# Performance work log

Measured on AMD Instinct MI355X. Metric: run time of the kernel, lower is better.

Reference implementation:

```python
import jax, jax.numpy as jnp
import numpy as np

N_NODES = 100000
N_EDGES = 800000
IN_DIM, HID_DIM, OUT_DIM = 128, 64, 7


def setup_inputs() -> dict:
    key = jax.random.key(0)
    ks = jax.random.split(key, 8)
    x = jax.random.normal(ks[0], (N_NODES, IN_DIM), dtype=jnp.float32)
    edge_index = jax.random.randint(ks[1], (2, N_EDGES), 0, N_NODES, dtype=jnp.int64)
    # Glorot-ish init for weights, zeros for bias (PyG GCNConv default)
    def glorot(k, shape):
        lim = float(np.sqrt(6.0 / (shape[0] + shape[1])))
        return jax.random.uniform(k, shape, dtype=jnp.float32, minval=-lim, maxval=lim)
    return {
        "x": x,
        "edge_index": edge_index,
        "W1": glorot(ks[2], (IN_DIM, HID_DIM)),
        "b1": jnp.zeros((HID_DIM,), jnp.float32),
        "W2": glorot(ks[3], (HID_DIM, HID_DIM)),
        "b2": jnp.zeros((HID_DIM,), jnp.float32),
        "W3": glorot(ks[4], (HID_DIM, OUT_DIM)),
        "b3": jnp.zeros((OUT_DIM,), jnp.float32),
    }


def _gcn_conv(h_in, src, dst, W, b, n_nodes):
    # PyG GCNConv: h = x @ W; add self-loops; D^-1/2 A_hat D^-1/2 aggregation; + b
    h = h_in @ W  # [N, F_out]
    # degree over destination nodes, +1 for self-loop
    deg = jax.ops.segment_sum(jnp.ones_like(dst, dtype=h.dtype), dst,
                              num_segments=n_nodes) + 1.0
    dinv = jax.lax.rsqrt(deg)  # [N]
    coef = dinv[src] * dinv[dst]  # [E]
    msg = h[src] * coef[:, None]  # gather + scale  [E, F_out]
    out = jax.ops.segment_sum(msg, dst, num_segments=n_nodes)  # scatter-add
    out = out + h * (dinv * dinv)[:, None]  # self-loop contribution
    return out + b


def reference(x, edge_index, W1, b1, W2, b2, W3, b3):
    src, dst = edge_index[0], edge_index[1]
    n = x.shape[0]
    h = jax.nn.relu(_gcn_conv(x, src, dst, W1, b1, n))
    # dropout(p=0.5) is identity in eval mode
    h = jax.nn.relu(_gcn_conv(h, src, dst, W2, b2, n))
    return _gcn_conv(h, src, dst, W3, b3, n)
```

## Files before the change

kernel.cpp:

```cpp
#include <hip/hip_runtime.h>

#define N_NODES 100000
#define N_EDGES 800000
#define IN_DIM 128
#define HID 64
#define OUT_DIM 7
#define CAP 32
#define NGROUP 8
#define DSLICE (N_NODES / NGROUP)
#define SUBBLK 390

typedef __bf16 vbf8 __attribute__((ext_vector_type(8)));
typedef float  vf4  __attribute__((ext_vector_type(4)));

#define GEMM_BLKS ((N_NODES / 16 + 3) / 4)
#define FILL_BLKS (NGROUP * SUBBLK)
#define SWZ2_BLKS 16
#define PH1_BLKS (GEMM_BLKS + FILL_BLKS + SWZ2_BLKS + 1)

__device__ __forceinline__ void wswz_body(int idx, const float* __restrict__ W,
                                          __bf16* __restrict__ out) {
    int j  = idx & 7;
    int l  = (idx >> 3) & 63;
    int nt = (idx >> 9) & 3;
    int ks = idx >> 11;
    int k  = ks * 32 + ((l >> 4) << 3) + j;
    int n  = nt * 16 + (l & 15);
    out[idx] = (__bf16)W[k * 64 + n];
}

__device__ __forceinline__ void gemm1_body(int g, int tid, const float* __restrict__ X,
                                           const float* __restrict__ W1,
                                           __bf16* __restrict__ Hb) {
    constexpr int K = IN_DIM, KS = K / 32;
    const int lane = tid & 63;
    const int w = g * 4 + (tid >> 6);
    if (w >= N_NODES / 16) return;
    const int r0 = w * 16;
    const int m = lane & 15;
    const int quad = lane >> 4;

    vbf8 bfrag[KS][4];
    #pragma unroll
    for (int ks = 0; ks < KS; ++ks)
        #pragma unroll
        for (int nt = 0; nt < 4; ++nt)
            #pragma unroll
            for (int j = 0; j < 8; ++j)
                bfrag[ks][nt][j] = (__bf16)W1[(ks * 32 + quad * 8 + j) * 64 + nt * 16 + m];

    vf4 acc[4] = {};
    #pragma unroll
    for (int ks = 0; ks < KS; ++ks) {
        const float* xp = X + (size_t)(r0 + m) * K + ks * 32 + quad * 8;
        float4 f0 = *(const float4*)xp;
        float4 f1 = *(const float4*)(xp + 4);
        vbf8 a;
        a[0] = (__bf16)f0.x; a[1] = (__bf16)f0.y; a[2] = (__bf16)f0.z; a[3] = (__bf16)f0.w;
        a[4] = (__bf16)f1.x; a[5] = (__bf16)f1.y; a[6] = (__bf16)f1.z; a[7] = (__bf16)f1.w;
        #pragma unroll
        for (int nt = 0; nt < 4; ++nt)
            acc[nt] = __builtin_amdgcn_mfma_f32_16x16x32_bf16(a, bfrag[ks][nt], acc[nt], 0, 0, 0);
    }
    #pragma unroll
    for (int nt = 0; nt < 4; ++nt)
        #pragma unroll
        for (int r = 0; r < 4; ++r)
            Hb[(size_t)(r0 + quad * 4 + r) * 64 + nt * 16 + m] = (__bf16)acc[nt][r];
}

__device__ __forceinline__ void fill_body(int bb, int tid, const int* __restrict__ ei,
                                          int* __restrict__ cnt, int* __restrict__ csr) {
    int group = bb & 7, sub = bb >> 3;
    int lo = group * DSLICE;
    const int4* dst4 = (const int4*)(ei + N_EDGES);
    const int4* src4 = (const int4*)ei;
    for (int e4 = sub * 256 + tid; e4 < N_EDGES / 4; e4 += SUBBLK * 256) {
        int4 d4 = dst4[e4];
        bool m0 = (unsigned)(d4.x - lo) < (unsigned)DSLICE;
        bool m1 = (unsigned)(d4.y - lo) < (unsigned)DSLICE;
        bool m2 = (unsigned)(d4.z - lo) < (unsigned)DSLICE;
        bool m3 = (unsigned)(d4.w - lo) < (unsigned)DSLICE;
        if (!(m0 | m1 | m2 | m3)) continue;
        int4 s4 = src4[e4];
        if (m0) { int p = atomicAdd(&cnt[d4.x], 1); if (p < CAP) csr[(size_t)d4.x * CAP + p] = s4.x; }
        if (m1) { int p = atomicAdd(&cnt[d4.y], 1); if (p < CAP) csr[(size_t)d4.y * CAP + p] = s4.y; }
        if (m2) { int p = atomicAdd(&cnt[d4.z], 1); if (p < CAP) csr[(size_t)d4.z * CAP + p] = s4.z; }
        if (m3) { int p = atomicAdd(&cnt[d4.w], 1); if (p < CAP) csr[(size_t)d4.w * CAP + p] = s4.w; }
    }
}

__global__ __launch_bounds__(256)
void k_phase1(const int* __restrict__ ei, int* __restrict__ cnt, int* __restrict__ csr,
              const float* __restrict__ X, const float* __restrict__ W1,
              const float* __restrict__ W2, __bf16* __restrict__ Wz2,
              __bf16* __restrict__ HbA, __bf16* __restrict__ HbB,
              float* __restrict__ S) {
    int b = blockIdx.x;
    if (b < GEMM_BLKS) { gemm1_body(b, threadIdx.x, X, W1, HbA); return; }
    b -= GEMM_BLKS;
    if (b < FILL_BLKS) { fill_body(b, threadIdx.x, ei, cnt, csr); return; }
    b -= FILL_BLKS;
    if (b < SWZ2_BLKS) { wswz_body(b * 256 + threadIdx.x, W2, Wz2); return; }
    int t = threadIdx.x;
    if (t < 32)       ((unsigned*)(HbA + (size_t)N_NODES * 64))[t] = 0u;
    else if (t < 64)  ((unsigned*)(HbB + (size_t)N_NODES * 64))[t - 32] = 0u;
    else if (t < 71)  S[(size_t)N_NODES * 7 + (t - 64)] = 0.0f;
}

__global__ __launch_bounds__(256)
void k_g64gemm2(const int* __restrict__ cnt, const int* __restrict__ csr,
                const float* __restrict__ bias, const __bf16* __restrict__ Hs,
                const __bf16* __restrict__ Wz2, __bf16* __restrict__ HbB) {
    __shared__ __bf16 tl[32][72];
    const int tid = threadIdx.x;
    const int nl = tid >> 3;
    const int q  = tid & 7;
    const int node = blockIdx.x * 32 + nl;

    int deg = cnt[node];
    int end = deg < CAP ? deg : CAP;
    float dd = rsqrtf((float)deg + 1.0f);
    vbf8 h8 = *(const vbf8*)(Hs + (size_t)node * 64 + q * 8);
    float acc[8];
    #pragma unroll
    for (int t = 0; t < 8; ++t) acc[t] = (float)h8[t] * dd;

    const int4* row4 = (const int4*)(csr + (size_t)node * CAP);
    int4 qa = row4[0], qb = row4[1], qc = row4[2], qd = row4[3];
    int srcs[16] = {qa.x, qa.y, qa.z, qa.w, qb.x, qb.y, qb.z, qb.w,
                    qc.x, qc.y, qc.z, qc.w, qd.x, qd.y, qd.z, qd.w};
    #pragma unroll
    for (int t = 0; t < 16; ++t) {
        int s = (t < end) ? srcs[t] : N_NODES;
        float ds = rsqrtf((float)cnt[s] + 1.0f);
        vbf8 v = *(const vbf8*)(Hs + (size_t)s * 64 + q * 8);
        #pragma unroll
        for (int u = 0; u < 8; ++u) acc[u] += (float)v[u] * ds;
    }
    for (int j = 16; j < end; ++j) {
        int s = (csr + (size_t)node * CAP)[j];
        float ds = rsqrtf((float)cnt[s] + 1.0f);
        vbf8 v = *(const vbf8*)(Hs + (size_t)s * 64 + q * 8);
        #pragma unroll
        for (int u = 0; u < 8; ++u) acc[u] += (float)v[u] * ds;
    }
    float4 b0 = *(const float4*)(bias + q * 8);
    float4 b1 = *(const float4*)(bias + q * 8 + 4);
    float bb[8] = {b0.x, b0.y, b0.z, b0.w, b1.x, b1.y, b1.z, b1.w};
    vbf8 o;
    #pragma unroll
    for (int t = 0; t < 8; ++t) o[t] = (__bf16)fmaxf(fmaf(acc[t], dd, bb[t]), 0.f);
    *(vbf8*)&tl[nl][q * 8] = o;
    __syncthreads();

    const int wave = tid >> 6;
    const int lane = tid & 63;
    const int m = lane & 15;
    const int quad = lane >> 4;
    const int tile = wave >> 1;
    const int nt0 = (wave & 1) * 2;

    vbf8 bfrag[2][2];
    const vbf8* wp = (const vbf8*)Wz2;
    #pragma unroll
    for (int ks = 0; ks < 2; ++ks)
        #pragma unroll
        for (int i = 0; i < 2; ++i)
            bfrag[ks][i] = wp[(ks * 4 + nt0 + i) * 64 + lane];

    vf4 acc2[2] = {};
    #pragma unroll
    for (int ks = 0; ks < 2; ++ks) {
        vbf8 a = *(const vbf8*)&tl[tile * 16 + m][ks * 32 + quad * 8];
        #pragma unroll
        for (int i = 0; i < 2; ++i)
            acc2[i] = __builtin_amdgcn_mfma_f32_16x16x32_bf16(a, bfrag[ks][i], acc2[i], 0, 0, 0);
    }
    const int gr0 = blockIdx.x * 32 + tile * 16;
    float dv[4];
    #pragma unroll
    for (int r = 0; r < 4; ++r)
        dv[r] = rsqrtf((float)cnt[gr0 + quad * 4 + r] + 1.0f);
    #pragma unroll
    for (int i = 0; i < 2; ++i)
        #pragma unroll
        for (int r = 0; r < 4; ++r)
            HbB[(size_t)(gr0 + quad * 4 + r) * 64 + (nt0 + i) * 16 + m] =
                (__bf16)(acc2[i][r] * dv[r]);
}

__global__ __launch_bounds__(256)
void k_gather64m(const int* __restrict__ cnt, const int* __restrict__ csr,
                 const float* __restrict__ bias, const __bf16* __restrict__ Hs,
                 const float* __restrict__ W3, float* __restrict__ S) {
    int node = blockIdx.x * 32 + (threadIdx.x >> 3);
    int q = threadIdx.x & 7;
    if (node >= N_NODES) return;
    int deg = cnt[node];
    int end = deg < CAP ? deg : CAP;
    float dd = rsqrtf((float)deg + 1.0f);
    vbf8 h8 = *(const vbf8*)(Hs + (size_t)node * 64 + q * 8);
    float acc[8];
    #pragma unroll
    for (int t = 0; t < 8; ++t) acc[t] = (float)h8[t];

    const int4* row4 = (const int4*)(csr + (size_t)node * CAP);
    int4 qa = row4[0], qb = row4[1], qc = row4[2], qd = row4[3];
    int srcs[16] = {qa.x, qa.y, qa.z, qa.w, qb.x, qb.y, qb.z, qb.w,
                    qc.x, qc.y, qc.z, qc.w, qd.x, qd.y, qd.z, qd.w};
    #pragma unroll
    for (int t = 0; t < 16; ++t) {
        int s = (t < end) ? srcs[t] : N_NODES;
        vbf8 v = *(const vbf8*)(Hs + (size_t)s * 64 + q * 8);
        #pragma unroll
        for (int u = 0; u < 8; ++u) acc[u] += (float)v[u];
    }
    for (int j = 16; j < end; ++j) {
        int s = (csr + (size_t)node * CAP)[j];
        vbf8 v = *(const vbf8*)(Hs + (size_t)s * 64 + q * 8);
        #pragma unroll
        for (int u = 0; u < 8; ++u) acc[u] += (float)v[u];
    }

    float4 b0 = *(const float4*)(bias + q * 8);
    float4 b1 = *(const float4*)(bias + q * 8 + 4);
    float bb[8] = {b0.x, b0.y, b0.z, b0.w, b1.x, b1.y, b1.z, b1.w};
    float p[7] = {};
    #pragma unroll
    for (int t = 0; t < 8; ++t) {
        float r = fmaxf(fmaf(acc[t], dd, bb[t]), 0.f);
        #pragma unroll
        for (int j = 0; j < 7; ++j)
            p[j] = fmaf(r, W3[(q * 8 + t) * 7 + j], p[j]);
    }
    #pragma unroll
    for (int msk = 1; msk < 8; msk <<= 1)
        #pragma unroll
        for (int j = 0; j < 7; ++j)
            p[j] += __shfl_xor(p[j], msk, 8);
    if (q < 7) {
        float v = p[0];
        if (q == 1) v = p[1]; else if (q == 2) v = p[2]; else if (q == 3) v = p[3];
        else if (q == 4) v = p[4]; else if (q == 5) v = p[5]; else if (q == 6) v = p[6];
        S[(size_t)node * 7 + q] = v * dd;
    }
}

__global__ __launch_bounds__(256)
void k_gather7(const int* __restrict__ cnt, const int* __restrict__ csr,
               const float* __restrict__ S, const float* __restrict__ b3,
               float* __restrict__ Out) {
    int node = blockIdx.x * 32 + (threadIdx.x >> 3);
    int j7 = threadIdx.x & 7;
    if (node >= N_NODES || j7 >= 7) return;
    int deg = cnt[node];
    int end = deg < CAP ? deg : CAP;
    float dd = rsqrtf((float)deg + 1.0f);
    const int4* row4 = (const int4*)(csr + (size_t)node * CAP);
    int4 qa = row4[0], qb = row4[1], qc = row4[2], qd = row4[3];
    int srcs[16] = {qa.x, qa.y, qa.z, qa.w, qb.x, qb.y, qb.z, qb.w,
                    qc.x, qc.y, qc.z, qc.w, qd.x, qd.y, qd.z, qd.w};
    float acc = S[(size_t)node * 7 + j7];
    #pragma unroll
    for (int t = 0; t < 16; ++t) {
        int s = (t < end) ? srcs[t] : N_NODES;
        acc += S[(size_t)s * 7 + j7];
    }
    for (int j = 16; j < end; ++j) {
        int s = (csr + (size_t)node * CAP)[j];
        acc += S[(size_t)s * 7 + j7];
    }
    Out[(size_t)node * 7 + j7] = fmaf(acc, dd, b3[j7]);
}

static inline size_t align256(size_t x) { return (x + 255) & ~(size_t)255; }

extern "C" void kernel_launch(void* const* d_in, const int* in_sizes, int n_in,
                              void* d_out, int out_size, void* d_ws, size_t ws_size,
                              hipStream_t stream) {
    const float* x  = (const float*)d_in[0];
    const int*   ei = (const int*)d_in[1];
    const float* W1 = (const float*)d_in[2];
    const float* b1 = (const float*)d_in[3];
    const float* W2 = (const float*)d_in[4];
    const float* b2 = (const float*)d_in[5];
    const float* W3 = (const float*)d_in[6];
    const float* b3 = (const float*)d_in[7];
    float* out = (float*)d_out;

    char* wsp = (char*)d_ws;
    int*    cnt  = (int*)wsp;    wsp += align256(sizeof(int) * (N_NODES + 1));
    int*    csr  = (int*)wsp;    wsp += align256(sizeof(int) * (size_t)N_NODES * CAP);
    __bf16* Wz2  = (__bf16*)wsp; wsp += align256(sizeof(__bf16) * HID * 64);
    __bf16* HbA  = (__bf16*)wsp; wsp += align256(sizeof(__bf16) * (size_t)(N_NODES + 1) * 64);
    __bf16* HbB  = (__bf16*)wsp; wsp += align256(sizeof(__bf16) * (size_t)(N_NODES + 1) * 64);
    float*  bufS = (float*)wsp;  wsp += align256(sizeof(float) * (size_t)(N_NODES + 1) * 7);

    hipMemsetAsync(cnt, 0, sizeof(int) * (N_NODES + 1), stream);
    k_phase1<<<PH1_BLKS, 256, 0, stream>>>(ei, cnt, csr, x, W1, W2, Wz2, HbA, HbB, bufS);
    k_g64gemm2<<<N_NODES / 32, 256, 0, stream>>>(cnt, csr, b1, HbA, Wz2, HbB);
    k_gather64m<<<N_NODES / 32, 256, 0, stream>>>(cnt, csr, b2, HbB, W3, bufS);
    k_gather7<<<N_NODES / 32, 256, 0, stream>>>(cnt, csr, bufS, b3, out);
}
```

Before: 209.2 us.

## Replace memset with init kernel that pre-swizzles W1 and batches fill atomics

A small init kernel now zeroes the degree counters, writes the padding rows and converts both W1 and W2 into the MFMA-swizzled bf16 layout, replacing the hipMemsetAsync call. The first GEMM then loads its B fragments as vector loads instead of doing 32 scalar strided fp32 loads and conversions per wave. The CSR fill issues all four atomics before doing the dependent stores, so the atomic latencies can overlap. The cost is one extra kernel launch in place of the memset.

```diff
diff --git a/kernel.cpp b/kernel.cpp
--- a/kernel.cpp
+++ b/kernel.cpp
@@ -15,8 +15,7 @@
 
 #define GEMM_BLKS ((N_NODES / 16 + 3) / 4)
 #define FILL_BLKS (NGROUP * SUBBLK)
-#define SWZ2_BLKS 16
-#define PH1_BLKS (GEMM_BLKS + FILL_BLKS + SWZ2_BLKS + 1)
+#define PH1_BLKS (GEMM_BLKS + FILL_BLKS)
 
 __device__ __forceinline__ void wswz_body(int idx, const float* __restrict__ W,
                                           __bf16* __restrict__ out) {
@@ -29,8 +28,29 @@
     out[idx] = (__bf16)W[k * 64 + n];
 }
 
+__global__ __launch_bounds__(256)
+void k_init(const float* __restrict__ W1, __bf16* __restrict__ Wz1,
+            const float* __restrict__ W2, __bf16* __restrict__ Wz2,
+            int* __restrict__ cnt,
+            __bf16* __restrict__ HbA, __bf16* __restrict__ HbB,
+            float* __restrict__ S) {
+    int b = blockIdx.x;
+    int t = threadIdx.x;
+    if (b < 32) { wswz_body(b * 256 + t, W1, Wz1); return; }
+    if (b < 48) { wswz_body((b - 32) * 256 + t, W2, Wz2); return; }
+    if (b < 147) {
+        int idx = (b - 48) * 256 + t;
+        if (idx < 25000)      ((int4*)cnt)[idx] = make_int4(0, 0, 0, 0);
+        else if (idx == 25000) cnt[N_NODES] = 0;
+        return;
+    }
+    if (t < 32)       ((unsigned*)(HbA + (size_t)N_NODES * 64))[t] = 0u;
+    else if (t < 64)  ((unsigned*)(HbB + (size_t)N_NODES * 64))[t - 32] = 0u;
+    else if (t < 71)  S[(size_t)N_NODES * 7 + (t - 64)] = 0.0f;
+}
+
 __device__ __forceinline__ void gemm1_body(int g, int tid, const float* __restrict__ X,
-                                           const float* __restrict__ W1,
+                                           const __bf16* __restrict__ Wswz,
                                            __bf16* __restrict__ Hb) {
     constexpr int K = IN_DIM, KS = K / 32;
     const int lane = tid & 63;
@@ -41,13 +61,12 @@
     const int quad = lane >> 4;
 
     vbf8 bfrag[KS][4];
+    const vbf8* wp = (const vbf8*)Wswz;
     #pragma unroll
     for (int ks = 0; ks < KS; ++ks)
         #pragma unroll
         for (int nt = 0; nt < 4; ++nt)
-            #pragma unroll
-            for (int j = 0; j < 8; ++j)
-                bfrag[ks][nt][j] = (__bf16)W1[(ks * 32 + quad * 8 + j) * 64 + nt * 16 + m];
+            bfrag[ks][nt] = wp[(ks * 4 + nt) * 64 + lane];
 
     vf4 acc[4] = {};
     #pragma unroll
@@ -83,29 +102,25 @@
         bool m3 = (unsigned)(d4.w - lo) < (unsigned)DSLICE;
         if (!(m0 | m1 | m2 | m3)) continue;
         int4 s4 = src4[e4];
-        if (m0) { int p = atomicAdd(&cnt[d4.x], 1); if (p < CAP) csr[(size_t)d4.x * CAP + p] = s4.x; }
-        if (m1) { int p = atomicAdd(&cnt[d4.y], 1); if (p < CAP) csr[(size_t)d4.y * CAP + p] = s4.y; }
-        if (m2) { int p = atomicAdd(&cnt[d4.z], 1); if (p < CAP) csr[(size_t)d4.z * CAP + p] = s4.z; }
-        if (m3) { int p = atomicAdd(&cnt[d4.w], 1); if (p < CAP) csr[(size_t)d4.w * CAP + p] = s4.w; }
+        int p0 = 0, p1 = 0, p2 = 0, p3 = 0;
+        if (m0) p0 = atomicAdd(&cnt[d4.x], 1);
+        if (m1) p1 = atomicAdd(&cnt[d4.y], 1);
+        if (m2) p2 = atomicAdd(&cnt[d4.z], 1);
+        if (m3) p3 = atomicAdd(&cnt[d4.w], 1);
+        if (m0 && p0 < CAP) csr[(size_t)d4.x * CAP + p0] = s4.x;
+        if (m1 && p1 < CAP) csr[(size_t)d4.y * CAP + p1] = s4.y;
+        if (m2 && p2 < CAP) csr[(size_t)d4.z * CAP + p2] = s4.z;
+        if (m3 && p3 < CAP) csr[(size_t)d4.w * CAP + p3] = s4.w;
     }
 }
 
 __global__ __launch_bounds__(256)
 void k_phase1(const int* __restrict__ ei, int* __restrict__ cnt, int* __restrict__ csr,
-              const float* __restrict__ X, const float* __restrict__ W1,
-              const float* __restrict__ W2, __bf16* __restrict__ Wz2,
-              __bf16* __restrict__ HbA, __bf16* __restrict__ HbB,
-              float* __restrict__ S) {
+              const float* __restrict__ X, const __bf16* __restrict__ Wz1,
+              __bf16* __restrict__ HbA) {
     int b = blockIdx.x;
-    if (b < GEMM_BLKS) { gemm1_body(b, threadIdx.x, X, W1, HbA); return; }
-    b -= GEMM_BLKS;
-    if (b < FILL_BLKS) { fill_body(b, threadIdx.x, ei, cnt, csr); return; }
-    b -= FILL_BLKS;
-    if (b < SWZ2_BLKS) { wswz_body(b * 256 + threadIdx.x, W2, Wz2); return; }
-    int t = threadIdx.x;
-    if (t < 32)       ((unsigned*)(HbA + (size_t)N_NODES * 64))[t] = 0u;
-    else if (t < 64)  ((unsigned*)(HbB + (size_t)N_NODES * 64))[t - 32] = 0u;
-    else if (t < 71)  S[(size_t)N_NODES * 7 + (t - 64)] = 0.0f;
+    if (b < GEMM_BLKS) gemm1_body(b, threadIdx.x, X, Wz1, HbA);
+    else               fill_body(b - GEMM_BLKS, threadIdx.x, ei, cnt, csr);
 }
 
 __global__ __launch_bounds__(256)
@@ -292,13 +307,14 @@
     char* wsp = (char*)d_ws;
     int*    cnt  = (int*)wsp;    wsp += align256(sizeof(int) * (N_NODES + 1));
     int*    csr  = (int*)wsp;    wsp += align256(sizeof(int) * (size_t)N_NODES * CAP);
+    __bf16* Wz1  = (__bf16*)wsp; wsp += align256(sizeof(__bf16) * IN_DIM * 64);
     __bf16* Wz2  = (__bf16*)wsp; wsp += align256(sizeof(__bf16) * HID * 64);
     __bf16* HbA  = (__bf16*)wsp; wsp += align256(sizeof(__bf16) * (size_t)(N_NODES + 1) * 64);
     __bf16* HbB  = (__bf16*)wsp; wsp += align256(sizeof(__bf16) * (size_t)(N_NODES + 1) * 64);
     float*  bufS = (float*)wsp;  wsp += align256(sizeof(float) * (size_t)(N_NODES + 1) * 7);
 
-    hipMemsetAsync(cnt, 0, sizeof(int) * (N_NODES + 1), stream);
-    k_phase1<<<PH1_BLKS, 256, 0, stream>>>(ei, cnt, csr, x, W1, W2, Wz2, HbA, HbB, bufS);
+    k_init<<<148, 256, 0, stream>>>(W1, Wz1, W2, Wz2, cnt, HbA, HbB, bufS);
+    k_phase1<<<PH1_BLKS, 256, 0, stream>>>(ei, cnt, csr, x, Wz1, HbA);
     k_g64gemm2<<<N_NODES / 32, 256, 0, stream>>>(cnt, csr, b1, HbA, Wz2, HbB);
     k_gather64m<<<N_NODES / 32, 256, 0, stream>>>(cnt, csr, b2, HbB, W3, bufS);
     k_gather7<<<N_NODES / 32, 256, 0, stream>>>(cnt, csr, bufS, b3, out);
```

After: 199.4 us. -4.7%, faster.
